# Kernel optimization log

Hardware: AMD Instinct MI355X
Metric: run time of the kernel (lower is better)

The kernel has to match this reference:

```python
import jax, jax.numpy as jnp
import numpy as np

B, S, D, H = 2, 2048, 768, 12
DK = D // H

def setup_inputs() -> dict:
    key = jax.random.key(0)
    ks = jax.random.split(key, 5)
    scale = 1.0 / np.sqrt(D)
    return {
        "X": jax.random.normal(ks[0], (B, S, D), dtype=jnp.float32),
        "Wq": jax.random.normal(ks[1], (D, D), dtype=jnp.float32) * scale,
        "Wk": jax.random.normal(ks[2], (D, D), dtype=jnp.float32) * scale,
        "Wv": jax.random.normal(ks[3], (D, D), dtype=jnp.float32) * scale,
        "Wo": jax.random.normal(ks[4], (D, D), dtype=jnp.float32) * scale,
    }

def reference(X, Wq, Wk, Wv, Wo):
    # torch Linear: y = x @ W.T  (no bias in this repo's Linear)
    Q = X @ Wq.T  # (B,S,D)
    K = X @ Wk.T
    V = X @ Wv.T
    def split_heads(t):
        return t.reshape(B, S, H, DK).transpose(0, 2, 1, 3)  # (B,H,S,DK)
    Qh, Kh, Vh = split_heads(Q), split_heads(K), split_heads(V)
    scores = jnp.einsum('bhqd,bhkd->bhqk', Qh, Kh) / jnp.sqrt(jnp.float32(DK))
    causal = jnp.tril(jnp.ones((S, S), dtype=bool))  # keep lower triangle
    scores = jnp.where(causal, scores, -jnp.inf)
    attn = jax.nn.softmax(scores, axis=-1)
    out_h = jnp.einsum('bhqk,bhkd->bhqd', attn, Vh)  # (B,H,S,DK)
    out = out_h.transpose(0, 2, 1, 3).reshape(B, S, D)
    return out @ Wo.T
```

## Files before the change

### kernel.cpp

```cpp
#include <hip/hip_runtime.h>
#include <stdint.h>

#define BB   2
#define SS   2048
#define DD   768
#define HH   12
#define MM   (BB*SS)
#define XSZ  (MM*DD)
#define WSZ  (DD*DD)

typedef __bf16 v8bf __attribute__((ext_vector_type(8)));
typedef float  v4f  __attribute__((ext_vector_type(4)));

__device__ inline v4f mfma16(v8bf a, v8bf b, v4f c) {
    return __builtin_amdgcn_mfma_f32_16x16x32_bf16(a, b, c, 0, 0, 0);
}

__device__ inline unsigned short f2bf(float f) {
    union { float f; uint32_t u; } v; v.f = f;
    return (unsigned short)((v.u + 0x7FFFu + ((v.u >> 16) & 1u)) >> 16);
}

__device__ inline uint4 cvt8(const float* __restrict__ p) {
    uint4 out;
    unsigned short* s = (unsigned short*)&out;
#pragma unroll
    for (int j = 0; j < 8; ++j) s[j] = f2bf(p[j]);
    return out;
}

__device__ __forceinline__ void gld_lds16(const unsigned short* g, unsigned short* l) {
    __builtin_amdgcn_global_load_lds(
        (const __attribute__((address_space(1))) void*)g,
        (__attribute__((address_space(3))) void*)l, 16, 0, 0);
}

__global__ __launch_bounds__(256) void cvt_w3(
    const float* __restrict__ Wq, const float* __restrict__ Wk,
    const float* __restrict__ Wv, unsigned short* __restrict__ dst)
{
    long i4 = ((long)blockIdx.x * 256 + threadIdx.x) * 4;
    int t = (int)(i4 / WSZ);
    long off = i4 - (long)t * WSZ;
    const float* s = (t == 0) ? Wq : (t == 1) ? Wk : Wv;
    float4 v = *(const float4*)(s + off);
    ushort4 o;
    o.x = f2bf(v.x); o.y = f2bf(v.y); o.z = f2bf(v.z); o.w = f2bf(v.w);
    *(ushort4*)(dst + (size_t)t * WSZ + off) = o;
}

__global__ __launch_bounds__(256) void cvt_wo(
    const float* __restrict__ Wo, unsigned short* __restrict__ dst)
{
    long i4 = ((long)blockIdx.x * 256 + threadIdx.x) * 4;
    float4 v = *(const float4*)(Wo + i4);
    ushort4 o;
    o.x = f2bf(v.x); o.y = f2bf(v.y); o.z = f2bf(v.z); o.w = f2bf(v.w);
    *(ushort4*)(dst + i4) = o;
}

__global__ __launch_bounds__(256) void gemm_qkv(
    const float* __restrict__ X,
    const unsigned short* __restrict__ Wq,
    const unsigned short* __restrict__ Wk,
    const unsigned short* __restrict__ Wv,
    unsigned short* __restrict__ Qo,
    unsigned short* __restrict__ Ko,
    unsigned short* __restrict__ Vo)
{
    __shared__ __align__(16) unsigned short As[64 * 64];
    __shared__ __align__(16) unsigned short Bs[3][64 * 64];

    const int flat = (int)(blockIdx.y * gridDim.x + blockIdx.x);
    const int sw   = (flat & 7) * 96 + (flat >> 3);
    const int m0   = (sw / 12) * 64;
    const int n0   = (sw % 12) * 64;

    const int tid  = threadIdx.x;
    const int wave = tid >> 6, lane = tid & 63;
    const int quad = lane >> 4, l16 = lane & 15;
    const int waveM = (wave >> 1) * 32, waveN = (wave & 1) * 32;

    const int rA  = tid >> 2;
    const int cA  = (tid & 3) * 16;
    const int rxA = (rA & 7) << 4;

    const int rB  = wave * 8 + (lane >> 3);
    const int cB  = ((lane & 7) ^ (lane >> 3)) * 8;

    const int swz = (l16 & 7) << 4;

    v4f acc[3][2][2] = {};

    const float* ap0 = X + (size_t)(m0 + rA) * DD + cA;
    const unsigned short* w0 = Wq + (size_t)(n0 + rB) * DD + cB;
    const unsigned short* w1 = Wk + (size_t)(n0 + rB) * DD + cB;
    const unsigned short* w2 = Wv + (size_t)(n0 + rB) * DD + cB;

    for (int kt = 0; kt < DD; kt += 64) {
        __syncthreads();
        *(uint4*)((char*)As + rA * 128 + ((cA * 2)      ^ rxA)) = cvt8(ap0 + kt);
        *(uint4*)((char*)As + rA * 128 + ((cA * 2 + 16) ^ rxA)) = cvt8(ap0 + kt + 8);
        gld_lds16(w0 + kt,           &Bs[0][wave * 512]);
        gld_lds16(w0 + kt + 32 * DD, &Bs[0][2048 + wave * 512]);
        gld_lds16(w1 + kt,           &Bs[1][wave * 512]);
        gld_lds16(w1 + kt + 32 * DD, &Bs[1][2048 + wave * 512]);
        gld_lds16(w2 + kt,           &Bs[2][wave * 512]);
        gld_lds16(w2 + kt + 32 * DD, &Bs[2][2048 + wave * 512]);
        __syncthreads();

        v8bf af[2][2];
#pragma unroll
        for (int mi = 0; mi < 2; ++mi) {
            const char* arow = (const char*)As + (size_t)(waveM + mi * 16 + l16) * 128;
#pragma unroll
            for (int kf = 0; kf < 2; ++kf)
                af[mi][kf] = *(const v8bf*)(arow + ((kf * 64 + quad * 16) ^ swz));
        }
#pragma unroll
        for (int z = 0; z < 3; ++z) {
            v8bf bfr[2][2];
#pragma unroll
            for (int ni = 0; ni < 2; ++ni) {
                const char* brow = (const char*)&Bs[z][0] + (size_t)(waveN + ni * 16 + l16) * 128;
#pragma unroll
                for (int kf = 0; kf < 2; ++kf)
                    bfr[ni][kf] = *(const v8bf*)(brow + ((kf * 64 + quad * 16) ^ swz));
            }
#pragma unroll
            for (int mi = 0; mi < 2; ++mi)
#pragma unroll
                for (int ni = 0; ni < 2; ++ni) {
                    acc[z][mi][ni] = mfma16(af[mi][0], bfr[ni][0], acc[z][mi][ni]);
                    acc[z][mi][ni] = mfma16(af[mi][1], bfr[ni][1], acc[z][mi][ni]);
                }
        }
    }

#pragma unroll
    for (int mi = 0; mi < 2; ++mi)
#pragma unroll
        for (int ni = 0; ni < 2; ++ni)
#pragma unroll
            for (int r = 0; r < 4; ++r) {
                const int row = m0 + waveM + mi * 16 + quad * 4 + r;
                const int col = n0 + waveN + ni * 16 + l16;
                Qo[(size_t)row * DD + col] = f2bf(acc[0][mi][ni][r]);
                Ko[(size_t)row * DD + col] = f2bf(acc[1][mi][ni][r]);
                const int b = row >> 11, s = row & 2047;
                const int h = col >> 6,  dk = col & 63;
                Vo[(((size_t)(b * HH + h)) * 64 + dk) * SS + s] = f2bf(acc[2][mi][ni][r]);
            }
}

template<int A_ASYNC, int W_ASYNC, int C_F32>
__global__ __launch_bounds__(256) void gemm_64(
    const void* __restrict__ Ain, const void* __restrict__ W0,
    void* __restrict__ C0)
{
    const int K = DD, N = DD;
    const void* W = W0;
    void* C = C0;

    __shared__ __align__(16) unsigned short As[64 * 32];
    __shared__ __align__(16) unsigned short Bs[64 * 32];

    const int tid  = threadIdx.x;
    const int wave = tid >> 6, lane = tid & 63;
    const int quad = lane >> 4, l16 = lane & 15;
    const int waveM = (wave >> 1) * 32, waveN = (wave & 1) * 32;
    const int m0 = blockIdx.y * 64, n0 = blockIdx.x * 64;

    const int rS = (tid >> 2), cS = (tid & 3) * 8;

    v4f acc[2][2] = {};

    for (int kt = 0; kt < K; kt += 32) {
        __syncthreads();
        if (A_ASYNC)
            gld_lds16((const unsigned short*)Ain + (size_t)(m0 + rS) * K + kt + cS,
                      &As[wave * 512]);
        else
            *(uint4*)(&As[tid * 8]) = cvt8((const float*)Ain + (size_t)(m0 + rS) * K + kt + cS);
        if (W_ASYNC)
            gld_lds16((const unsigned short*)W + (size_t)(n0 + rS) * K + kt + cS,
                      &Bs[wave * 512]);
        else
            *(uint4*)(&Bs[tid * 8]) = cvt8((const float*)W + (size_t)(n0 + rS) * K + kt + cS);
        __syncthreads();

        v8bf af[2], bf[2];
#pragma unroll
        for (int i = 0; i < 2; ++i) {
            af[i] = *(const v8bf*)(&As[(waveM + i * 16 + l16) * 32 + quad * 8]);
            bf[i] = *(const v8bf*)(&Bs[(waveN + i * 16 + l16) * 32 + quad * 8]);
        }
#pragma unroll
        for (int mi = 0; mi < 2; ++mi)
#pragma unroll
            for (int ni = 0; ni < 2; ++ni)
                acc[mi][ni] = mfma16(af[mi], bf[ni], acc[mi][ni]);
    }

#pragma unroll
    for (int mi = 0; mi < 2; ++mi)
#pragma unroll
        for (int ni = 0; ni < 2; ++ni)
#pragma unroll
            for (int r = 0; r < 4; ++r) {
                int row = m0 + waveM + mi * 16 + quad * 4 + r;
                int col = n0 + waveN + ni * 16 + l16;
                if (C_F32) {
                    ((float*)C)[(size_t)row * N + col] = acc[mi][ni][r];
                } else {
                    ((unsigned short*)C)[(size_t)row * N + col] = f2bf(acc[mi][ni][r]);
                }
            }
}

__global__ __launch_bounds__(256, 3) void attn_ls(
    const unsigned short* Q,
    const unsigned short* __restrict__ Kg,
    const unsigned short* __restrict__ Vt,
    unsigned short* O)
{
    const int h = blockIdx.x, b = blockIdx.y;
    const int qs = (SS / 64 - 1 - (int)blockIdx.z) * 64;
    const int tid  = threadIdx.x;
    const int wave = tid >> 6, lane = tid & 63;
    const int quad = lane >> 4, l16 = lane & 15;
    const int qw = qs + wave * 16;
    const float scale = 0.125f;

    __shared__ __align__(16) unsigned short Ks[2][4096];
    __shared__ __align__(16) unsigned short Vs[2][4096];
    __shared__ __align__(16) unsigned short Ps[4][16 * 72];

    v8bf qf0, qf1;
    {
        const unsigned short* qp = &Q[((size_t)(b * SS + qw + l16)) * DD + h * 64];
        qf0 = *(const v8bf*)(qp + quad * 8);
        qf1 = *(const v8bf*)(qp + 32 + quad * 8);
    }

    const int NT = qs / 64 + 1;
    const char* kgb = (const char*)&Kg[(size_t)(b * SS) * DD + h * 64];
    const char* vgb = (const char*)&Vt[((size_t)(b * HH + h) * 64) * SS];

    const int rA = wave * 8 + (lane >> 3);
    const int oA = ((lane & 7) * 16) ^ ((rA & 7) << 4);
    const int swz = (l16 & 7) << 4;

    v4f oacc[4] = {};
    float l_run[4] = {0.f, 0.f, 0.f, 0.f};
    unsigned short* pw = &Ps[wave][0];

    gld_lds16((const unsigned short*)(kgb + (size_t)rA        * (DD * 2) + oA), &Ks[0][wave * 512]);
    gld_lds16((const unsigned short*)(kgb + (size_t)(rA + 32) * (DD * 2) + oA), &Ks[0][2048 + wave * 512]);
    gld_lds16((const unsigned short*)(vgb + (size_t)rA        * (SS * 2) + oA), &Vs[0][wave * 512]);
    gld_lds16((const unsigned short*)(vgb + (size_t)(rA + 32) * (SS * 2) + oA), &Vs[0][2048 + wave * 512]);
    __syncthreads();

    for (int kt = 0; kt < NT; ++kt) {
        const int cur = kt & 1;
        const int kb  = kt * 64;

        if (kt + 1 < NT) {
            const size_t kb2 = (size_t)(kb + 64);
            gld_lds16((const unsigned short*)(kgb + (kb2 + rA)      * (DD * 2) + oA), &Ks[cur ^ 1][wave * 512]);
            gld_lds16((const unsigned short*)(kgb + (kb2 + rA + 32) * (DD * 2) + oA), &Ks[cur ^ 1][2048 + wave * 512]);
            gld_lds16((const unsigned short*)(vgb + (size_t)rA        * (SS * 2) + kb2 * 2 + oA), &Vs[cur ^ 1][wave * 512]);
            gld_lds16((const unsigned short*)(vgb + (size_t)(rA + 32) * (SS * 2) + kb2 * 2 + oA), &Vs[cur ^ 1][2048 + wave * 512]);
        }

        const char* ksb = (const char*)&Ks[cur][0];
        const char* vsb = (const char*)&Vs[cur][0];

        v8bf kf0[4], kf1[4];
#pragma unroll
        for (int nk = 0; nk < 4; ++nk) {
            const char* krow = ksb + (size_t)(nk * 16 + l16) * 128;
            kf0[nk] = *(const v8bf*)(krow + ((quad * 16) ^ swz));
            kf1[nk] = *(const v8bf*)(krow + ((64 + quad * 16) ^ swz));
        }

        v4f sacc[4] = {};
#pragma unroll
        for (int nk = 0; nk < 4; ++nk) {
            sacc[nk] = mfma16(qf0, kf0[nk], sacc[nk]);
            sacc[nk] = mfma16(qf1, kf1[nk], sacc[nk]);
        }

        const bool diag = (kt == NT - 1);
        float pv[4][4];
#pragma unroll
        for (int nk = 0; nk < 4; ++nk)
#pragma unroll
            for (int r = 0; r < 4; ++r) {
                float p = __expf(sacc[nk][r] * scale);
                if (diag) {
                    int key  = kb + nk * 16 + l16;
                    int qrow = qw + quad * 4 + r;
                    if (key > qrow) p = 0.0f;
                }
                pv[nk][r] = p;
                l_run[r] += p;
            }

        v8bf vf[2][4];
#pragma unroll
        for (int kc = 0; kc < 2; ++kc)
#pragma unroll
            for (int dt = 0; dt < 4; ++dt) {
                const char* vr = vsb + (size_t)(dt * 16 + l16) * 128;
                vf[kc][dt] = *(const v8bf*)(vr + ((kc * 64 + quad * 16) ^ swz));
            }

#pragma unroll
        for (int nk = 0; nk < 4; ++nk)
#pragma unroll
            for (int r = 0; r < 4; ++r)
                pw[(quad * 4 + r) * 72 + nk * 16 + l16] = f2bf(pv[nk][r]);
        __asm__ volatile("" ::: "memory");

        v8bf pa0 = *(const v8bf*)(&pw[l16 * 72 + quad * 8]);
        v8bf pa1 = *(const v8bf*)(&pw[l16 * 72 + 32 + quad * 8]);
#pragma unroll
        for (int dt = 0; dt < 4; ++dt) oacc[dt] = mfma16(pa0, vf[0][dt], oacc[dt]);
#pragma unroll
        for (int dt = 0; dt < 4; ++dt) oacc[dt] = mfma16(pa1, vf[1][dt], oacc[dt]);

        __syncthreads();
    }

    for (int off = 1; off < 16; off <<= 1)
#pragma unroll
        for (int r = 0; r < 4; ++r)
            l_run[r] += __shfl_xor(l_run[r], off, 64);

    float inv[4];
#pragma unroll
    for (int r = 0; r < 4; ++r) inv[r] = 1.0f / l_run[r];

    unsigned short* ob = &O[((size_t)(b * SS + qw + quad * 4)) * DD + h * 64 + l16];
#pragma unroll
    for (int r = 0; r < 4; ++r)
#pragma unroll
        for (int dt = 0; dt < 4; ++dt)
            ob[(size_t)r * DD + dt * 16] = f2bf(oacc[dt][r] * inv[r]);
}

extern "C" void kernel_launch(void* const* d_in, const int* in_sizes, int n_in,
                              void* d_out, int out_size, void* d_ws, size_t ws_size,
                              hipStream_t stream)
{
    const float* X  = (const float*)d_in[0];
    const float* Wq = (const float*)d_in[1];
    const float* Wk = (const float*)d_in[2];
    const float* Wv = (const float*)d_in[3];
    const float* Wo = (const float*)d_in[4];
    float* Out = (float*)d_out;

    unsigned short* Qb  = (unsigned short*)d_ws;
    unsigned short* Kb  = Qb + XSZ;
    unsigned short* Vtb = (unsigned short*)d_out;
    unsigned short* Wqb = Vtb + XSZ;
    unsigned short* Wkb = Wqb + WSZ;
    unsigned short* Wvb = Wkb + WSZ;

    dim3 blk(256);
    cvt_w3<<<1728, blk, 0, stream>>>(Wq, Wk, Wv, Wqb);

    dim3 g1(DD / 64, MM / 64);
    gemm_qkv<<<g1, blk, 0, stream>>>(X, Wqb, Wkb, Wvb, Qb, Kb, Vtb);

    dim3 g2(HH, BB, SS / 64);
    attn_ls<<<g2, blk, 0, stream>>>(Qb, Kb, Vtb, Qb);

    cvt_wo<<<576, blk, 0, stream>>>(Wo, Kb);

    dim3 g3(DD / 64, MM / 64);
    gemm_64<1, 1, 1><<<g3, blk, 0, stream>>>(Qb, Kb, Out);
}
```

Measured before the change: 158.8 us.

## Pre-convert X to bf16 and use 128x128 tiles for fused QKV GEMM

```diff
diff --git a/kernel.cpp b/kernel.cpp
--- a/kernel.cpp
+++ b/kernel.cpp
@@ -33,6 +33,26 @@
     __builtin_amdgcn_global_load_lds(
         (const __attribute__((address_space(1))) void*)g,
         (__attribute__((address_space(3))) void*)l, 16, 0, 0);
+}
+
+__global__ __launch_bounds__(256) void cvt_x3(
+    const float* __restrict__ Wq, const float* __restrict__ Wk,
+    const float* __restrict__ Wv, const float* __restrict__ X,
+    unsigned short* __restrict__ Wqb,
+    unsigned short* __restrict__ Xb)
+{
+    long i4 = ((long)blockIdx.x * 256 + threadIdx.x) * 4;
+    const float* s; unsigned short* d; long off;
+    if (i4 < 3L * WSZ) {
+        int t = (int)(i4 / WSZ); off = i4 - (long)t * WSZ;
+        s = (t == 0) ? Wq : (t == 1) ? Wk : Wv; d = Wqb + (size_t)t * WSZ;
+    } else {
+        off = i4 - 3L * WSZ; s = X; d = Xb;
+    }
+    float4 v = *(const float4*)(s + off);
+    ushort4 o;
+    o.x = f2bf(v.x); o.y = f2bf(v.y); o.z = f2bf(v.z); o.w = f2bf(v.w);
+    *(ushort4*)(d + off) = o;
 }
 
 __global__ __launch_bounds__(256) void cvt_w3(
@@ -48,7 +68,6 @@
     o.x = f2bf(v.x); o.y = f2bf(v.y); o.z = f2bf(v.z); o.w = f2bf(v.w);
     *(ushort4*)(dst + (size_t)t * WSZ + off) = o;
 }
-
 __global__ __launch_bounds__(256) void cvt_wo(
     const float* __restrict__ Wo, unsigned short* __restrict__ dst)
 {
@@ -59,7 +78,88 @@
     *(ushort4*)(dst + i4) = o;
 }
 
-__global__ __launch_bounds__(256) void gemm_qkv(
+__global__ __launch_bounds__(256) void gemm_qkv128(
+    const unsigned short* __restrict__ Xb,
+    const unsigned short* __restrict__ Wq,
+    const unsigned short* __restrict__ Wk,
+    const unsigned short* __restrict__ Wv,
+    unsigned short* __restrict__ Qo,
+    unsigned short* __restrict__ Ko,
+    unsigned short* __restrict__ Vo)
+{
+    __shared__ __align__(16) unsigned short As[128 * 64];
+    __shared__ __align__(16) unsigned short Bs[128 * 64];
+
+    const int flat = (int)(blockIdx.y * gridDim.x + blockIdx.x);
+    const int sw   = (flat & 7) * 72 + (flat >> 3);
+    const int m0   = (sw / 18) * 128;
+    const int ncat = (sw % 18) * 128;
+    const int z    = ncat / DD;
+    const int n0   = ncat - z * DD;
+
+    const unsigned short* W = (z == 0) ? Wq : (z == 1) ? Wk : Wv;
+
+    const int tid  = threadIdx.x;
+    const int wave = tid >> 6, lane = tid & 63;
+    const int quad = lane >> 4, l16 = lane & 15;
+    const int waveM = (wave >> 1) * 64, waveN = (wave & 1) * 64;
+
+    const int rB  = wave * 8 + (lane >> 3);
+    const int cB  = ((lane & 7) ^ (lane >> 3)) * 8;
+    const int swz = (l16 & 7) << 4;
+
+    v4f acc[4][4] = {};
+
+    const unsigned short* a0 = Xb + (size_t)(m0 + rB) * DD + cB;
+    const unsigned short* b0 = W  + (size_t)(n0 + rB) * DD + cB;
+
+    for (int kt = 0; kt < DD; kt += 64) {
+        __syncthreads();
+#pragma unroll
+        for (int c = 0; c < 4; ++c) {
+            gld_lds16(a0 + kt + (size_t)(c * 32) * DD, &As[c * 2048 + wave * 512]);
+            gld_lds16(b0 + kt + (size_t)(c * 32) * DD, &Bs[c * 2048 + wave * 512]);
+        }
+        __syncthreads();
+
+#pragma unroll
+        for (int kf = 0; kf < 2; ++kf) {
+            v8bf af[4], bfr[4];
+#pragma unroll
+            for (int i = 0; i < 4; ++i) {
+                af[i]  = *(const v8bf*)((const char*)As +
+                          (size_t)(waveM + i * 16 + l16) * 128 + ((kf * 64 + quad * 16) ^ swz));
+                bfr[i] = *(const v8bf*)((const char*)Bs +
+                          (size_t)(waveN + i * 16 + l16) * 128 + ((kf * 64 + quad * 16) ^ swz));
+            }
+#pragma unroll
+            for (int mi = 0; mi < 4; ++mi)
+#pragma unroll
+                for (int ni = 0; ni < 4; ++ni)
+                    acc[mi][ni] = mfma16(af[mi], bfr[ni], acc[mi][ni]);
+        }
+    }
+
+#pragma unroll
+    for (int mi = 0; mi < 4; ++mi)
+#pragma unroll
+        for (int ni = 0; ni < 4; ++ni)
+#pragma unroll
+            for (int r = 0; r < 4; ++r) {
+                const int row = m0 + waveM + mi * 16 + quad * 4 + r;
+                const int col = n0 + waveN + ni * 16 + l16;
+                const unsigned short val = f2bf(acc[mi][ni][r]);
+                if (z == 0)      Qo[(size_t)row * DD + col] = val;
+                else if (z == 1) Ko[(size_t)row * DD + col] = val;
+                else {
+                    const int b = row >> 11, s = row & 2047;
+                    const int h = col >> 6,  dk = col & 63;
+                    Vo[(((size_t)(b * HH + h)) * 64 + dk) * SS + s] = val;
+                }
+            }
+}
+
+__global__ __launch_bounds__(256) void gemm_qkv64(
     const float* __restrict__ X,
     const unsigned short* __restrict__ Wq,
     const unsigned short* __restrict__ Wk,
@@ -87,7 +187,6 @@
 
     const int rB  = wave * 8 + (lane >> 3);
     const int cB  = ((lane & 7) ^ (lane >> 3)) * 8;
-
     const int swz = (l16 & 7) << 4;
 
     v4f acc[3][2][2] = {};
@@ -363,22 +462,37 @@
 
     unsigned short* Qb  = (unsigned short*)d_ws;
     unsigned short* Kb  = Qb + XSZ;
+    unsigned short* Xb  = Kb + XSZ;
     unsigned short* Vtb = (unsigned short*)d_out;
     unsigned short* Wqb = Vtb + XSZ;
     unsigned short* Wkb = Wqb + WSZ;
     unsigned short* Wvb = Wkb + WSZ;
 
     dim3 blk(256);
-    cvt_w3<<<1728, blk, 0, stream>>>(Wq, Wk, Wv, Wqb);
-
-    dim3 g1(DD / 64, MM / 64);
-    gemm_qkv<<<g1, blk, 0, stream>>>(X, Wqb, Wkb, Wvb, Qb, Kb, Vtb);
-
     dim3 g2(HH, BB, SS / 64);
-    attn_ls<<<g2, blk, 0, stream>>>(Qb, Kb, Vtb, Qb);
-
-    cvt_wo<<<576, blk, 0, stream>>>(Wo, Kb);
-
     dim3 g3(DD / 64, MM / 64);
-    gemm_64<1, 1, 1><<<g3, blk, 0, stream>>>(Qb, Kb, Out);
-}
+
+    if (ws_size >= (size_t)8 * XSZ) {
+        cvt_x3<<<4800, blk, 0, stream>>>(Wq, Wk, Wv, X, Wqb, Xb);
+
+        dim3 g1(2304 / 128, MM / 128);
+        gemm_qkv128<<<g1, blk, 0, stream>>>(Xb, Wqb, Wkb, Wvb, Qb, Kb, Vtb);
+
+        attn_ls<<<g2, blk, 0, stream>>>(Qb, Kb, Vtb, Qb);
+
+        cvt_wo<<<576, blk, 0, stream>>>(Wo, Kb);
+
+        gemm_64<1, 1, 1><<<g3, blk, 0, stream>>>(Qb, Kb, Out);
+    } else {
+        cvt_w3<<<1728, blk, 0, stream>>>(Wq, Wk, Wv, Wqb);
+
+        dim3 g1(DD / 64, MM / 64);
+        gemm_qkv64<<<g1, blk, 0, stream>>>(X, Wqb, Wkb, Wvb, Qb, Kb, Vtb);
+
+        attn_ls<<<g2, blk, 0, stream>>>(Qb, Kb, Vtb, Qb);
+
+        cvt_wo<<<576, blk, 0, stream>>>(Wo, Kb);
+
+        gemm_64<1, 1, 1><<<g3, blk, 0, stream>>>(Qb, Kb, Out);
+    }
+}
```

After: 173.8 us. +9.5%, slower.

## Fuse weight bf16 conversion into GEMMs and double-buffer output projection

Applied to the files above, without the earlier changes.

```diff
diff --git a/kernel.cpp b/kernel.cpp
--- a/kernel.cpp
+++ b/kernel.cpp
@@ -35,35 +35,11 @@
         (__attribute__((address_space(3))) void*)l, 16, 0, 0);
 }
 
-__global__ __launch_bounds__(256) void cvt_w3(
-    const float* __restrict__ Wq, const float* __restrict__ Wk,
-    const float* __restrict__ Wv, unsigned short* __restrict__ dst)
-{
-    long i4 = ((long)blockIdx.x * 256 + threadIdx.x) * 4;
-    int t = (int)(i4 / WSZ);
-    long off = i4 - (long)t * WSZ;
-    const float* s = (t == 0) ? Wq : (t == 1) ? Wk : Wv;
-    float4 v = *(const float4*)(s + off);
-    ushort4 o;
-    o.x = f2bf(v.x); o.y = f2bf(v.y); o.z = f2bf(v.z); o.w = f2bf(v.w);
-    *(ushort4*)(dst + (size_t)t * WSZ + off) = o;
-}
-
-__global__ __launch_bounds__(256) void cvt_wo(
-    const float* __restrict__ Wo, unsigned short* __restrict__ dst)
-{
-    long i4 = ((long)blockIdx.x * 256 + threadIdx.x) * 4;
-    float4 v = *(const float4*)(Wo + i4);
-    ushort4 o;
-    o.x = f2bf(v.x); o.y = f2bf(v.y); o.z = f2bf(v.z); o.w = f2bf(v.w);
-    *(ushort4*)(dst + i4) = o;
-}
-
-__global__ __launch_bounds__(256) void gemm_qkv(
+__global__ __launch_bounds__(256) void gemm_qkv64f(
     const float* __restrict__ X,
-    const unsigned short* __restrict__ Wq,
-    const unsigned short* __restrict__ Wk,
-    const unsigned short* __restrict__ Wv,
+    const float* __restrict__ Wq,
+    const float* __restrict__ Wk,
+    const float* __restrict__ Wv,
     unsigned short* __restrict__ Qo,
     unsigned short* __restrict__ Ko,
     unsigned short* __restrict__ Vo)
@@ -84,29 +60,25 @@
     const int rA  = tid >> 2;
     const int cA  = (tid & 3) * 16;
     const int rxA = (rA & 7) << 4;
-
-    const int rB  = wave * 8 + (lane >> 3);
-    const int cB  = ((lane & 7) ^ (lane >> 3)) * 8;
-
     const int swz = (l16 & 7) << 4;
 
     v4f acc[3][2][2] = {};
 
-    const float* ap0 = X + (size_t)(m0 + rA) * DD + cA;
-    const unsigned short* w0 = Wq + (size_t)(n0 + rB) * DD + cB;
-    const unsigned short* w1 = Wk + (size_t)(n0 + rB) * DD + cB;
-    const unsigned short* w2 = Wv + (size_t)(n0 + rB) * DD + cB;
+    const float* ap = X  + (size_t)(m0 + rA) * DD + cA;
+    const float* w0 = Wq + (size_t)(n0 + rA) * DD + cA;
+    const float* w1 = Wk + (size_t)(n0 + rA) * DD + cA;
+    const float* w2 = Wv + (size_t)(n0 + rA) * DD + cA;
 
     for (int kt = 0; kt < DD; kt += 64) {
         __syncthreads();
-        *(uint4*)((char*)As + rA * 128 + ((cA * 2)      ^ rxA)) = cvt8(ap0 + kt);
-        *(uint4*)((char*)As + rA * 128 + ((cA * 2 + 16) ^ rxA)) = cvt8(ap0 + kt + 8);
-        gld_lds16(w0 + kt,           &Bs[0][wave * 512]);
-        gld_lds16(w0 + kt + 32 * DD, &Bs[0][2048 + wave * 512]);
-        gld_lds16(w1 + kt,           &Bs[1][wave * 512]);
-        gld_lds16(w1 + kt + 32 * DD, &Bs[1][2048 + wave * 512]);
-        gld_lds16(w2 + kt,           &Bs[2][wave * 512]);
-        gld_lds16(w2 + kt + 32 * DD, &Bs[2][2048 + wave * 512]);
+        *(uint4*)((char*)As + rA * 128 + ((cA * 2)      ^ rxA)) = cvt8(ap + kt);
+        *(uint4*)((char*)As + rA * 128 + ((cA * 2 + 16) ^ rxA)) = cvt8(ap + kt + 8);
+        *(uint4*)((char*)&Bs[0][0] + rA * 128 + ((cA * 2)      ^ rxA)) = cvt8(w0 + kt);
+        *(uint4*)((char*)&Bs[0][0] + rA * 128 + ((cA * 2 + 16) ^ rxA)) = cvt8(w0 + kt + 8);
+        *(uint4*)((char*)&Bs[1][0] + rA * 128 + ((cA * 2)      ^ rxA)) = cvt8(w1 + kt);
+        *(uint4*)((char*)&Bs[1][0] + rA * 128 + ((cA * 2 + 16) ^ rxA)) = cvt8(w1 + kt + 8);
+        *(uint4*)((char*)&Bs[2][0] + rA * 128 + ((cA * 2)      ^ rxA)) = cvt8(w2 + kt);
+        *(uint4*)((char*)&Bs[2][0] + rA * 128 + ((cA * 2 + 16) ^ rxA)) = cvt8(w2 + kt + 8);
         __syncthreads();
 
         v8bf af[2][2];
@@ -153,53 +125,68 @@
             }
 }
 
-template<int A_ASYNC, int W_ASYNC, int C_F32>
-__global__ __launch_bounds__(256) void gemm_64(
-    const void* __restrict__ Ain, const void* __restrict__ W0,
-    void* __restrict__ C0)
+__global__ __launch_bounds__(256) void gemm_of(
+    const unsigned short* __restrict__ A,
+    const float* __restrict__ W,
+    float* __restrict__ C)
 {
-    const int K = DD, N = DD;
-    const void* W = W0;
-    void* C = C0;
-
-    __shared__ __align__(16) unsigned short As[64 * 32];
-    __shared__ __align__(16) unsigned short Bs[64 * 32];
+    __shared__ __align__(16) unsigned short As[2][64 * 64];
+    __shared__ __align__(16) unsigned short Bs[2][64 * 64];
+
+    const int flat = (int)(blockIdx.y * gridDim.x + blockIdx.x);
+    const int sw   = (flat & 7) * 96 + (flat >> 3);
+    const int m0   = (sw / 12) * 64;
+    const int n0   = (sw % 12) * 64;
 
     const int tid  = threadIdx.x;
     const int wave = tid >> 6, lane = tid & 63;
     const int quad = lane >> 4, l16 = lane & 15;
     const int waveM = (wave >> 1) * 32, waveN = (wave & 1) * 32;
-    const int m0 = blockIdx.y * 64, n0 = blockIdx.x * 64;
-
-    const int rS = (tid >> 2), cS = (tid & 3) * 8;
+
+    const int rB  = wave * 8 + (lane >> 3);
+    const int cB  = ((lane & 7) ^ (lane >> 3)) * 8;
+    const int rW  = tid >> 2;
+    const int cW  = (tid & 3) * 16;
+    const int rxW = (rW & 7) << 4;
+    const int swz = (l16 & 7) << 4;
+
+    const unsigned short* a0 = A + (size_t)(m0 + rB) * DD + cB;
+    const float*          b0 = W + (size_t)(n0 + rW) * DD + cW;
 
     v4f acc[2][2] = {};
 
-    for (int kt = 0; kt < K; kt += 32) {
+    gld_lds16(a0,           &As[0][wave * 512]);
+    gld_lds16(a0 + 32 * DD, &As[0][2048 + wave * 512]);
+    *(uint4*)((char*)&Bs[0][0] + rW * 128 + ((cW * 2)      ^ rxW)) = cvt8(b0);
+    *(uint4*)((char*)&Bs[0][0] + rW * 128 + ((cW * 2 + 16) ^ rxW)) = cvt8(b0 + 8);
+    __syncthreads();
+
+    int cur = 0;
+    for (int kt = 0; kt < DD; kt += 64) {
+        if (kt + 64 < DD) {
+            gld_lds16(a0 + kt + 64,           &As[cur ^ 1][wave * 512]);
+            gld_lds16(a0 + kt + 64 + 32 * DD, &As[cur ^ 1][2048 + wave * 512]);
+            *(uint4*)((char*)&Bs[cur ^ 1][0] + rW * 128 + ((cW * 2)      ^ rxW)) = cvt8(b0 + kt + 64);
+            *(uint4*)((char*)&Bs[cur ^ 1][0] + rW * 128 + ((cW * 2 + 16) ^ rxW)) = cvt8(b0 + kt + 64 + 8);
+        }
+#pragma unroll
+        for (int kf = 0; kf < 2; ++kf) {
+            v8bf af[2], bfr[2];
+#pragma unroll
+            for (int i = 0; i < 2; ++i) {
+                af[i]  = *(const v8bf*)((const char*)&As[cur][0] +
+                          (size_t)(waveM + i * 16 + l16) * 128 + ((kf * 64 + quad * 16) ^ swz));
+                bfr[i] = *(const v8bf*)((const char*)&Bs[cur][0] +
+                          (size_t)(waveN + i * 16 + l16) * 128 + ((kf * 64 + quad * 16) ^ swz));
+            }
+#pragma unroll
+            for (int mi = 0; mi < 2; ++mi)
+#pragma unroll
+                for (int ni = 0; ni < 2; ++ni)
+                    acc[mi][ni] = mfma16(af[mi], bfr[ni], acc[mi][ni]);
+        }
         __syncthreads();
-        if (A_ASYNC)
-            gld_lds16((const unsigned short*)Ain + (size_t)(m0 + rS) * K + kt + cS,
-                      &As[wave * 512]);
-        else
-            *(uint4*)(&As[tid * 8]) = cvt8((const float*)Ain + (size_t)(m0 + rS) * K + kt + cS);
-        if (W_ASYNC)
-            gld_lds16((const unsigned short*)W + (size_t)(n0 + rS) * K + kt + cS,
-                      &Bs[wave * 512]);
-        else
-            *(uint4*)(&Bs[tid * 8]) = cvt8((const float*)W + (size_t)(n0 + rS) * K + kt + cS);
-        __syncthreads();
-
-        v8bf af[2], bf[2];
-#pragma unroll
-        for (int i = 0; i < 2; ++i) {
-            af[i] = *(const v8bf*)(&As[(waveM + i * 16 + l16) * 32 + quad * 8]);
-            bf[i] = *(const v8bf*)(&Bs[(waveN + i * 16 + l16) * 32 + quad * 8]);
-        }
-#pragma unroll
-        for (int mi = 0; mi < 2; ++mi)
-#pragma unroll
-            for (int ni = 0; ni < 2; ++ni)
-                acc[mi][ni] = mfma16(af[mi], bf[ni], acc[mi][ni]);
+        cur ^= 1;
     }
 
 #pragma unroll
@@ -208,13 +195,9 @@
         for (int ni = 0; ni < 2; ++ni)
 #pragma unroll
             for (int r = 0; r < 4; ++r) {
-                int row = m0 + waveM + mi * 16 + quad * 4 + r;
-                int col = n0 + waveN + ni * 16 + l16;
-                if (C_F32) {
-                    ((float*)C)[(size_t)row * N + col] = acc[mi][ni][r];
-                } else {
-                    ((unsigned short*)C)[(size_t)row * N + col] = f2bf(acc[mi][ni][r]);
-                }
+                const int row = m0 + waveM + mi * 16 + quad * 4 + r;
+                const int col = n0 + waveN + ni * 16 + l16;
+                C[(size_t)row * DD + col] = acc[mi][ni][r];
             }
 }
 
@@ -364,21 +347,15 @@
     unsigned short* Qb  = (unsigned short*)d_ws;
     unsigned short* Kb  = Qb + XSZ;
     unsigned short* Vtb = (unsigned short*)d_out;
-    unsigned short* Wqb = Vtb + XSZ;
-    unsigned short* Wkb = Wqb + WSZ;
-    unsigned short* Wvb = Wkb + WSZ;
 
     dim3 blk(256);
-    cvt_w3<<<1728, blk, 0, stream>>>(Wq, Wk, Wv, Wqb);
 
     dim3 g1(DD / 64, MM / 64);
-    gemm_qkv<<<g1, blk, 0, stream>>>(X, Wqb, Wkb, Wvb, Qb, Kb, Vtb);
+    gemm_qkv64f<<<g1, blk, 0, stream>>>(X, Wq, Wk, Wv, Qb, Kb, Vtb);
 
     dim3 g2(HH, BB, SS / 64);
     attn_ls<<<g2, blk, 0, stream>>>(Qb, Kb, Vtb, Qb);
 
-    cvt_wo<<<576, blk, 0, stream>>>(Wo, Kb);
-
     dim3 g3(DD / 64, MM / 64);
-    gemm_64<1, 1, 1><<<g3, blk, 0, stream>>>(Qb, Kb, Out);
-}
+    gemm_of<<<g3, blk, 0, stream>>>(Qb, Wo, Out);
+}
```

Result: slower. 166.5 us (+4.8%).
